# Kernel tuning notes

Measured on AMD Instinct MI355X. Metric: run time of the kernel, lower is better.

## Reference

```python
import jax, jax.numpy as jnp
import numpy as np

B, T, D_IN = 256, 250, 700
H1, H2, D_OUT = 256, 256, 20
B_J0 = 0.01
BETA = 1.8  # adaptation strength (isAdapt=1)
LENS, SCALE, HIGHT, GAMMA = 0.5, 6.0, 0.15, 0.5
SQRT_2PI = float(np.sqrt(2.0 * np.pi))


def _gaussian(x, mu, sigma):
    return jnp.exp(-((x - mu) ** 2) / (2.0 * sigma ** 2)) / (SQRT_2PI * sigma)


@jax.custom_vjp
def act_fun(x):
    # Heaviside spike with multi-Gaussian surrogate gradient (gradient_type='MG')
    return (x > 0).astype(x.dtype)


def _act_fwd(x):
    return act_fun(x), x


def _act_bwd(x, g):
    temp = (_gaussian(x, 0.0, LENS) * (1.0 + HIGHT)
            - _gaussian(x, LENS, SCALE * LENS) * HIGHT
            - _gaussian(x, -LENS, SCALE * LENS) * HIGHT)
    return (g * temp * GAMMA,)


act_fun.defvjp(_act_fwd, _act_bwd)


def setup_inputs() -> dict:
    key = jax.random.key(0)
    ks = jax.random.split(key, 16)
    # binary-ish spike input (SHD spike trains), rand fill
    x = (jax.random.uniform(ks[0], (B, T, D_IN)) < 0.1).astype(jnp.float32)

    def xavier(k, out_d, in_d):
        lim = float(np.sqrt(6.0 / (in_d + out_d)))
        return jax.random.uniform(k, (out_d, in_d), jnp.float32, -lim, lim)

    return {
        "x": x,
        "w_i2h1": xavier(ks[1], H1, D_IN),
        "w_h12h1": xavier(ks[2], H1, H1),
        "w_h12h2": xavier(ks[3], H2, H1),
        "w_h22h2": xavier(ks[4], H2, H2),
        "w_h2o": xavier(ks[5], D_OUT, H2),
        "b_h1": jnp.zeros((H1,), jnp.float32),
        "b_h2": jnp.zeros((H2,), jnp.float32),
        "b_o": jnp.zeros((D_OUT,), jnp.float32),
        "tau_adp_h1": 150.0 + 10.0 * jax.random.normal(ks[6], (H1,), jnp.float32),
        "tau_adp_h2": 150.0 + 10.0 * jax.random.normal(ks[7], (H2,), jnp.float32),
        "tau_m_h1": 20.0 + 5.0 * jax.random.normal(ks[8], (H1,), jnp.float32),
        "tau_m_h2": 20.0 + 5.0 * jax.random.normal(ks[9], (H2,), jnp.float32),
        "tau_m_o": 20.0 + 5.0 * jax.random.normal(ks[10], (D_OUT,), jnp.float32),
    }


def _lif_step(inp, mem, spk, b, alpha, ro):
    # mem_update_adp with params=None, dparams=None, isAdapt=1, dt=1, R_m=1
    b = ro * b + BETA * (1.0 - ro) * spk
    mem = mem * alpha - b * spk + (1.0 - alpha) * inp
    spk = act_fun(mem - b - B_J0)
    return mem, spk, b


def reference(x, w_i2h1, w_h12h1, w_h12h2, w_h22h2, w_h2o,
              b_h1, b_h2, b_o, tau_adp_h1, tau_adp_h2,
              tau_m_h1, tau_m_h2, tau_m_o):
    bsz = x.shape[0]
    h1, h2, d_out = w_i2h1.shape[0], w_h12h2.shape[0], w_h2o.shape[0]

    alpha1 = jnp.exp(-1.0 / tau_m_h1)
    ro1 = jnp.exp(-1.0 / tau_adp_h1)
    alpha2 = jnp.exp(-1.0 / tau_m_h2)
    ro2 = jnp.exp(-1.0 / tau_adp_h2)
    alpha_o = jnp.exp(-1.0 / tau_m_o)

    init = (
        jnp.zeros((bsz, h1)), jnp.zeros((bsz, h1)), jnp.full((bsz, h1), B_J0),
        jnp.zeros((bsz, h2)), jnp.zeros((bsz, h2)), jnp.full((bsz, h2), B_J0),
        jnp.zeros((bsz, d_out)), jnp.zeros((bsz, d_out)),
    )
    xT = jnp.swapaxes(x, 0, 1)  # [T, B, D_in]

    def step(carry, xt):
        mem1, spk1, bb1, mem2, spk2, bb2, mem_o, acc = carry
        h1_in = xt @ w_i2h1.T + spk1 @ w_h12h1.T + b_h1
        mem1, spk1, bb1 = _lif_step(h1_in, mem1, spk1, bb1, alpha1, ro1)
        h2_in = spk1 @ w_h12h2.T + spk2 @ w_h22h2.T + b_h2
        mem2, spk2, bb2 = _lif_step(h2_in, mem2, spk2, bb2, alpha2, ro2)
        o_in = spk2 @ w_h2o.T + b_o
        mem_o = mem_o * alpha_o + (1.0 - alpha_o) * o_in  # output_Neuron
        acc = acc + jax.nn.softmax(mem_o, axis=-1)
        return (mem1, spk1, bb1, mem2, spk2, bb2, mem_o, acc), None

    carry, _ = jax.lax.scan(step, init, xT)
    return carry[-1]  # accumulated softmax over the 250 timesteps, [B, 20]
```

## Files before the change

kernel.cpp:

```cpp
#include <hip/hip_runtime.h>
#include <cstdint>
#include <cstddef>

#define BB 256
#define TT 250
#define DIN 700
#define H1 256
#define H2 256
#define DOUT 20
#define BJ0 0.01f
#define BETAC 1.8f
#define IQSCALE 3.814697265625e-06f

typedef float f32x4 __attribute__((ext_vector_type(4)));
typedef int   i32x4 __attribute__((ext_vector_type(4)));

#define COFF_BL  180224
#define SOFF_T11 180224
#define SOFF_T12 245760
#define SOFF_T22 311296
#define FOFF_W2O 188416
#define FOFF_XP  193536
#define FOFF_MO  16577536
#define N_TRANS  381952

#define BARRIER_LDS() asm volatile("s_waitcnt lgkmcnt(0)\n\ts_barrier" ::: "memory")

__device__ __forceinline__ short q18(float w) {
    float s = w * 262144.0f;
    s = fminf(fmaxf(s, -32767.0f), 32767.0f);
    return (short)__float2int_rn(s);
}

__global__ void transpose_all_k(const float* __restrict__ w_i2h1,
                                const float* __restrict__ w_h12h1,
                                const float* __restrict__ w_h12h2,
                                const float* __restrict__ w_h22h2,
                                const float* __restrict__ w_h2o,
                                signed char* __restrict__ cws,
                                short* __restrict__ sws,
                                float* __restrict__ fws) {
    int i = blockIdx.x * blockDim.x + threadIdx.x;
    if (i < 180224) {
        int h = i / 704, k = i - h * 704;
        int q = (k < DIN) ? (int)q18(w_i2h1[h * DIN + k]) : 0;
        q = q > 32639 ? 32639 : (q < -32640 ? -32640 : q);
        int hi = (q + 128) >> 8;
        int lo = q - (hi << 8);
        cws[i] = (signed char)hi;
        cws[COFF_BL + i] = (signed char)lo;
        return;
    }
    i -= 180224;
    if (i < 65536) { int d = i >> 8, h = i & 255;
        sws[SOFF_T11 + i] = q18(w_h12h1[h * H1 + d]); return; }
    i -= 65536;
    if (i < 65536) { int d = i >> 8, h = i & 255;
        sws[SOFF_T12 + i] = q18(w_h12h2[h * H1 + d]); return; }
    i -= 65536;
    if (i < 65536) { int d = i >> 8, h = i & 255;
        sws[SOFF_T22 + i] = q18(w_h22h2[h * H2 + d]); return; }
    i -= 65536;
    if (i < 5120)  { int j = i / 20, o = i % 20;
        fws[FOFF_W2O + i] = w_h2o[o * H2 + j]; return; }
}

__global__ __launch_bounds__(256) void xgemm_k(const float* __restrict__ x,
                                               const signed char* __restrict__ Bh,
                                               const signed char* __restrict__ Bl,
                                               const float* __restrict__ b_h1,
                                               float* __restrict__ Xp) {
    const int t    = threadIdx.x;
    const int lane = t & 63;
    const int w    = t >> 6;
    const int m0   = blockIdx.x * 32;

    __shared__ __align__(16) signed char Asub[32 * 720];
    __shared__ __align__(16) signed char Bhs[256 * 80];
    __shared__ __align__(16) signed char Bls[256 * 80];

    #pragma unroll
    for (int it = 0; it < 22; ++it) {
        int flat = it * 256 + t;
        int row  = flat / 176;
        int c4   = flat - row * 176;
        unsigned int pk = 0u;
        if (c4 < 175) {
            const float* xr = x + (size_t)(m0 + row) * DIN;
            float4 f = *(const float4*)(xr + (c4 << 2));
            pk = (f.x != 0.f ? 1u : 0u)
               | (f.y != 0.f ? 1u : 0u) << 8
               | (f.z != 0.f ? 1u : 0u) << 16
               | (f.w != 0.f ? 1u : 0u) << 24;
        }
        *(unsigned int*)(Asub + row * 720 + (c4 << 2)) = pk;
    }

    i32x4 acch[2][4], accl[2][4];
    #pragma unroll
    for (int mt = 0; mt < 2; ++mt)
        #pragma unroll
        for (int nt = 0; nt < 4; ++nt) {
            acch[mt][nt] = (i32x4){0, 0, 0, 0};
            accl[mt][nt] = (i32x4){0, 0, 0, 0};
        }

    const int arow  = lane & 15;
    const int kg16  = (lane >> 4) << 4;
    const int bcol0 = w << 6;

    for (int ks = 0; ks < 11; ++ks) {
        __syncthreads();
        #pragma unroll
        for (int it2 = 0; it2 < 4; ++it2) {
            int row = it2 * 64 + (t >> 2);
            int ch  = (t & 3) << 4;
            int go  = row * 704 + ks * 64 + ch;
            *(int4*)(Bhs + row * 80 + ch) = *(const int4*)(Bh + go);
            *(int4*)(Bls + row * 80 + ch) = *(const int4*)(Bl + go);
        }
        __syncthreads();

        const int ko = ks * 64 + kg16;
        i32x4 a0 = *(const i32x4*)(Asub + arow * 720 + ko);
        i32x4 a1 = *(const i32x4*)(Asub + (16 + arow) * 720 + ko);
        #pragma unroll
        for (int nt = 0; nt < 4; ++nt) {
            const int bb = (bcol0 + nt * 16 + arow) * 80 + kg16;
            i32x4 bhf = *(const i32x4*)(Bhs + bb);
            i32x4 blf = *(const i32x4*)(Bls + bb);
            acch[0][nt] = __builtin_amdgcn_mfma_i32_16x16x64_i8(a0, bhf, acch[0][nt], 0, 0, 0);
            acch[1][nt] = __builtin_amdgcn_mfma_i32_16x16x64_i8(a1, bhf, acch[1][nt], 0, 0, 0);
            accl[0][nt] = __builtin_amdgcn_mfma_i32_16x16x64_i8(a0, blf, accl[0][nt], 0, 0, 0);
            accl[1][nt] = __builtin_amdgcn_mfma_i32_16x16x64_i8(a1, blf, accl[1][nt], 0, 0, 0);
        }
    }

    const int crb = (lane >> 4) << 2;
    #pragma unroll
    for (int nt = 0; nt < 4; ++nt) {
        int col = bcol0 + nt * 16 + arow;
        float bias = b_h1[col];
        #pragma unroll
        for (int mt = 0; mt < 2; ++mt) {
            #pragma unroll
            for (int r = 0; r < 4; ++r) {
                int row = m0 + mt * 16 + crb + r;
                int ir = (acch[mt][nt][r] << 8) + accl[mt][nt][r];
                __builtin_nontemporal_store(bias + (float)ir * IQSCALE,
                                            Xp + (size_t)row * H1 + col);
            }
        }
    }
}

__global__ __launch_bounds__(512) void rec_k(
    const float* __restrict__ Xp,
    const short* __restrict__ sT11, const short* __restrict__ sT12,
    const short* __restrict__ sT22, const float* __restrict__ wT2o,
    const float* __restrict__ b_h2, const float* __restrict__ b_o,
    const float* __restrict__ tau_adp_h1, const float* __restrict__ tau_adp_h2,
    const float* __restrict__ tau_m_h1, const float* __restrict__ tau_m_h2,
    const float* __restrict__ tau_m_o,
    float* __restrict__ Mo) {
    const int tid  = threadIdx.x;
    const int lane = tid & 63;
    const int w    = tid >> 6;
    const bool isL1 = (w < 4);
    const int c    = ((w & 3) << 6) + lane;
    const int b    = blockIdx.x;
    const float* __restrict__ XpB = Xp + (size_t)b * TT * H1;
    float* __restrict__ MoB = Mo + (size_t)b * TT * DOUT;

    __shared__ __align__(16) short sT22L[65536];
    __shared__ __align__(16) float w2oL[5120];
    __shared__ __align__(16) int lst1s[2][256];
    __shared__ __align__(16) int lst2s[2][256];
    __shared__ __align__(16) int lcnt[4][2];

    {
        const int* src = (const int*)sT22;
        int* dst = (int*)sT22L;
        for (int k = tid; k < 32768; k += 512) dst[k] = src[k];
        for (int k = tid; k < 5120; k += 512) w2oL[k] = wT2o[k];
        if (tid < 256) { lst1s[0][tid] = 0; lst1s[1][tid] = 0;
                         lst2s[0][tid] = 0; lst2s[1][tid] = 0; }
        if (tid < 8) ((int*)lcnt)[tid] = 0;
    }

    float alpha, rr, inb = 0.f;
    if (isL1) {
        alpha = expf(-1.0f / tau_m_h1[c]);
        rr    = expf(-1.0f / tau_adp_h1[c]);
    } else {
        alpha = expf(-1.0f / tau_m_h2[c]);
        rr    = expf(-1.0f / tau_adp_h2[c]);
        inb   = b_h2[c];
    }
    const int oc  = ((w & 3) * 5) + lane;
    const int ocs = (isL1 && lane < 5) ? oc : 0;
    float alpo = 0.f, bov = 0.f;
    if (isL1 && lane < 5) { alpo = expf(-1.0f / tau_m_o[oc]); bov = b_o[oc]; }

    float mem = 0.f, spk = 0.f, bbv = BJ0;
    float memo = 0.f;

    float xp_cur = 0.f;
    if (isL1) xp_cur = __builtin_nontemporal_load(XpB + c);
    __syncthreads();

    for (int i = 0; i <= TT + 1; ++i) {
        const int cur = i & 1, nxt = cur ^ 1;
        const int cc = i & 3, cn = (i + 1) & 3, cz = (i + 2) & 3;

        const int tot1 = lcnt[cc][0];
        const int tot2 = lcnt[cc][1];
        if (tid == 0) { lcnt[cz][0] = 0; lcnt[cz][1] = 0; }

        float xp_nxt = 0.f;
        if (isL1 && i + 1 < TT)
            xp_nxt = __builtin_nontemporal_load(XpB + (size_t)(i + 1) * H1 + c);

        const int* __restrict__ L1l = lst1s[cur];
        const int* __restrict__ L2l = lst2s[cur];

        int acc1 = 0, acc2 = 0;
        float ao = 0.f;

        if (isL1) {
            if (i < TT) {
                const short* colT = sT11 + c;
                int nb = tot1 >> 2, rem = tot1 & 3;
                for (int kk = 0; kk < nb; ++kk) {
                    int4 e = *(const int4*)(L1l + (kk << 2));
                    acc1 += colT[e.x << 8]; acc1 += colT[e.y << 8];
                    acc1 += colT[e.z << 8]; acc1 += colT[e.w << 8];
                }
                if (rem) {
                    int4 e = *(const int4*)(L1l + (nb << 2));
                    acc1 += colT[e.x << 8];
                    if (rem > 1) acc1 += colT[e.y << 8];
                    if (rem > 2) acc1 += colT[e.z << 8];
                }
            }
            if (i >= 2) {
                int nb = tot2 >> 2, rem = tot2 & 3;
                for (int kk = 0; kk < nb; ++kk) {
                    int4 e = *(const int4*)(L2l + (kk << 2));
                    float v0 = w2oL[e.x * DOUT + ocs];
                    float v1 = w2oL[e.y * DOUT + ocs];
                    float v2 = w2oL[e.z * DOUT + ocs];
                    float v3 = w2oL[e.w * DOUT + ocs];
                    ao += (v0 + v1) + (v2 + v3);
                }
                if (rem) {
                    int4 e = *(const int4*)(L2l + (nb << 2));
                    ao += w2oL[e.x * DOUT + ocs];
                    if (rem > 1) ao += w2oL[e.y * DOUT + ocs];
                    if (rem > 2) ao += w2oL[e.z * DOUT + ocs];
                }
            }
        } else if (i >= 1 && i <= TT) {
            {
                const short* colT = sT12 + c;
                int nb = tot1 >> 2, rem = tot1 & 3;
                for (int kk = 0; kk < nb; ++kk) {
                    int4 e = *(const int4*)(L1l + (kk << 2));
                    acc1 += colT[e.x << 8]; acc1 += colT[e.y << 8];
                    acc1 += colT[e.z << 8]; acc1 += colT[e.w << 8];
                }
                if (rem) {
                    int4 e = *(const int4*)(L1l + (nb << 2));
                    acc1 += colT[e.x << 8];
                    if (rem > 1) acc1 += colT[e.y << 8];
                    if (rem > 2) acc1 += colT[e.z << 8];
                }
            }
            {
                const short* colL = sT22L + c;
                int nb = tot2 >> 2, rem = tot2 & 3;
                for (int kk = 0; kk < nb; ++kk) {
                    int4 e = *(const int4*)(L2l + (kk << 2));
                    acc2 += colL[e.x << 8]; acc2 += colL[e.y << 8];
                    acc2 += colL[e.z << 8]; acc2 += colL[e.w << 8];
                }
                if (rem) {
                    int4 e = *(const int4*)(L2l + (nb << 2));
                    acc2 += colL[e.x << 8];
                    if (rem > 1) acc2 += colL[e.y << 8];
                    if (rem > 2) acc2 += colL[e.z << 8];
                }
            }
        }

        if (isL1) {
            if (i < TT) {
                float r1 = (float)acc1 * IQSCALE;
                bbv = rr * bbv + BETAC * (1.f - rr) * spk;
                mem = mem * alpha - bbv * spk + (1.f - alpha) * (xp_cur + r1);
                float ns = (mem - bbv - BJ0) > 0.f ? 1.f : 0.f;
                spk = ns;
                unsigned long long m = __ballot(ns != 0.f ? 1 : 0);
                int base = 0;
                if (lane == 0) base = atomicAdd(&lcnt[cn][0], __popcll(m));
                base = __shfl(base, 0);
                if (ns != 0.f)
                    lst1s[nxt][base + __popcll(m & ((1ull << lane) - 1ull))] = c;
            }
            if (lane < 5 && i >= 2) {
                memo = memo * alpo + (1.f - alpo) * (bov + ao);
                __builtin_nontemporal_store(memo, MoB + (size_t)(i - 2) * DOUT + oc);
            }
        } else if (i >= 1 && i <= TT) {
            float r23 = (float)(acc1 + acc2) * IQSCALE;
            bbv = rr * bbv + BETAC * (1.f - rr) * spk;
            mem = mem * alpha - bbv * spk + (1.f - alpha) * (inb + r23);
            float ns = (mem - bbv - BJ0) > 0.f ? 1.f : 0.f;
            spk = ns;
            unsigned long long m = __ballot(ns != 0.f ? 1 : 0);
            int base = 0;
            if (lane == 0) base = atomicAdd(&lcnt[cn][1], __popcll(m));
            base = __shfl(base, 0);
            if (ns != 0.f)
                lst2s[nxt][base + __popcll(m & ((1ull << lane) - 1ull))] = c;
        }

        BARRIER_LDS();
        xp_cur = xp_nxt;
    }
}

__global__ __launch_bounds__(256) void soft_k(const float* __restrict__ Mo,
                                              float* __restrict__ out) {
    const int b = blockIdx.x;
    const int t = threadIdx.x;
    __shared__ float sm[TT][DOUT];

    if (t < TT) {
        const float* row = Mo + ((size_t)b * TT + t) * DOUT;
        float v[DOUT];
        #pragma unroll
        for (int k = 0; k < DOUT; k += 4) {
            float4 r = *(const float4*)(row + k);
            v[k] = r.x; v[k + 1] = r.y; v[k + 2] = r.z; v[k + 3] = r.w;
        }
        float mx = v[0];
        #pragma unroll
        for (int j = 1; j < DOUT; ++j) mx = fmaxf(mx, v[j]);
        float s = 0.f;
        #pragma unroll
        for (int j = 0; j < DOUT; ++j) { v[j] = __expf(v[j] - mx); s += v[j]; }
        float inv = 1.0f / s;
        #pragma unroll
        for (int j = 0; j < DOUT; ++j) sm[t][j] = v[j] * inv;
    }
    __syncthreads();
    if (t < DOUT) {
        float acc = 0.f;
        for (int tt = 0; tt < TT; ++tt) acc += sm[tt][t];
        out[b * DOUT + t] = acc;
    }
}

extern "C" void kernel_launch(void* const* d_in, const int* in_sizes, int n_in,
                              void* d_out, int out_size, void* d_ws, size_t ws_size,
                              hipStream_t stream) {
    const float* x          = (const float*)d_in[0];
    const float* w_i2h1     = (const float*)d_in[1];
    const float* w_h12h1    = (const float*)d_in[2];
    const float* w_h12h2    = (const float*)d_in[3];
    const float* w_h22h2    = (const float*)d_in[4];
    const float* w_h2o      = (const float*)d_in[5];
    const float* b_h1       = (const float*)d_in[6];
    const float* b_h2       = (const float*)d_in[7];
    const float* b_o        = (const float*)d_in[8];
    const float* tau_adp_h1 = (const float*)d_in[9];
    const float* tau_adp_h2 = (const float*)d_in[10];
    const float* tau_m_h1   = (const float*)d_in[11];
    const float* tau_m_h2   = (const float*)d_in[12];
    const float* tau_m_o    = (const float*)d_in[13];

    signed char* cws = (signed char*)d_ws;
    short* sws = (short*)d_ws;
    float* fws = (float*)d_ws;
    const signed char* Bh = cws;
    const signed char* Bl = cws + COFF_BL;
    const short* sT11 = sws + SOFF_T11;
    const short* sT12 = sws + SOFF_T12;
    const short* sT22 = sws + SOFF_T22;
    float* wT2o = fws + FOFF_W2O;
    float* Xp   = fws + FOFF_XP;
    float* Mo   = fws + FOFF_MO;

    transpose_all_k<<<N_TRANS / 256, 256, 0, stream>>>(
        w_i2h1, w_h12h1, w_h12h2, w_h22h2, w_h2o, cws, sws, fws);

    xgemm_k<<<(BB * TT) / 32, 256, 0, stream>>>(x, Bh, Bl, b_h1, Xp);

    rec_k<<<BB, 512, 0, stream>>>(Xp, sT11, sT12, sT22, wT2o,
                                  b_h2, b_o, tau_adp_h1, tau_adp_h2,
                                  tau_m_h1, tau_m_h2, tau_m_o, Mo);

    soft_k<<<BB, 256, 0, stream>>>(Mo, (float*)d_out);
}
```

Baseline: 689.6 us.

## Replace LDS spike index lists with per-wave ballot bitmasks

Each wave now writes its 64-bit ballot mask of spiking neurons to LDS, replacing the atomic-counter compacted index lists. Consumers read the four masks into scalar registers with readfirstlane and walk the set bits with ctz to gather weight columns. This removes the LDS atomics, shuffles, scattered list writes and int4 list loads from each timestep. In exchange the gather loops become scalar bit-scan loops with a dependent ctz per spike and less unrolling.

```diff
diff --git a/kernel.cpp b/kernel.cpp
--- a/kernel.cpp
+++ b/kernel.cpp
@@ -30,6 +30,12 @@
     float s = w * 262144.0f;
     s = fminf(fmaxf(s, -32767.0f), 32767.0f);
     return (short)__float2int_rn(s);
+}
+
+__device__ __forceinline__ unsigned long long rfl64(unsigned long long m) {
+    unsigned lo = __builtin_amdgcn_readfirstlane((unsigned)m);
+    unsigned hi = __builtin_amdgcn_readfirstlane((unsigned)(m >> 32));
+    return ((unsigned long long)hi << 32) | lo;
 }
 
 __global__ void transpose_all_k(const float* __restrict__ w_i2h1,
@@ -174,18 +180,16 @@
 
     __shared__ __align__(16) short sT22L[65536];
     __shared__ __align__(16) float w2oL[5120];
-    __shared__ __align__(16) int lst1s[2][256];
-    __shared__ __align__(16) int lst2s[2][256];
-    __shared__ __align__(16) int lcnt[4][2];
+    __shared__ unsigned long long wm1[2][4];
+    __shared__ unsigned long long wm2[2][4];
 
     {
         const int* src = (const int*)sT22;
         int* dst = (int*)sT22L;
         for (int k = tid; k < 32768; k += 512) dst[k] = src[k];
         for (int k = tid; k < 5120; k += 512) w2oL[k] = wT2o[k];
-        if (tid < 256) { lst1s[0][tid] = 0; lst1s[1][tid] = 0;
-                         lst2s[0][tid] = 0; lst2s[1][tid] = 0; }
-        if (tid < 8) ((int*)lcnt)[tid] = 0;
+        if (tid < 8) wm1[tid >> 2][tid & 3] = 0ULL;
+        else if (tid < 16) wm2[(tid - 8) >> 2][tid & 3] = 0ULL;
     }
 
     float alpha, rr, inb = 0.f;
@@ -211,18 +215,17 @@
 
     for (int i = 0; i <= TT + 1; ++i) {
         const int cur = i & 1, nxt = cur ^ 1;
-        const int cc = i & 3, cn = (i + 1) & 3, cz = (i + 2) & 3;
-
-        const int tot1 = lcnt[cc][0];
-        const int tot2 = lcnt[cc][1];
-        if (tid == 0) { lcnt[cz][0] = 0; lcnt[cz][1] = 0; }
 
         float xp_nxt = 0.f;
         if (isL1 && i + 1 < TT)
             xp_nxt = __builtin_nontemporal_load(XpB + (size_t)(i + 1) * H1 + c);
 
-        const int* __restrict__ L1l = lst1s[cur];
-        const int* __restrict__ L2l = lst2s[cur];
+        unsigned long long M1[4], M2[4];
+        #pragma unroll
+        for (int q = 0; q < 4; ++q) {
+            M1[q] = rfl64(wm1[cur][q]);
+            M2[q] = rfl64(wm2[cur][q]);
+        }
 
         int acc1 = 0, acc2 = 0;
         float ao = 0.f;
@@ -230,99 +233,84 @@
         if (isL1) {
             if (i < TT) {
                 const short* colT = sT11 + c;
-                int nb = tot1 >> 2, rem = tot1 & 3;
-                for (int kk = 0; kk < nb; ++kk) {
-                    int4 e = *(const int4*)(L1l + (kk << 2));
-                    acc1 += colT[e.x << 8]; acc1 += colT[e.y << 8];
-                    acc1 += colT[e.z << 8]; acc1 += colT[e.w << 8];
+                #pragma unroll
+                for (int q = 0; q < 4; ++q) {
+                    unsigned long long m = M1[q];
+                    const int base = q << 6;
+                    while (m) {
+                        int j = __builtin_ctzll(m);
+                        m &= m - 1;
+                        acc1 += colT[(base + j) << 8];
+                    }
                 }
-                if (rem) {
-                    int4 e = *(const int4*)(L1l + (nb << 2));
-                    acc1 += colT[e.x << 8];
-                    if (rem > 1) acc1 += colT[e.y << 8];
-                    if (rem > 2) acc1 += colT[e.z << 8];
-                }
-            }
-            if (i >= 2) {
-                int nb = tot2 >> 2, rem = tot2 & 3;
-                for (int kk = 0; kk < nb; ++kk) {
-                    int4 e = *(const int4*)(L2l + (kk << 2));
-                    float v0 = w2oL[e.x * DOUT + ocs];
-                    float v1 = w2oL[e.y * DOUT + ocs];
-                    float v2 = w2oL[e.z * DOUT + ocs];
-                    float v3 = w2oL[e.w * DOUT + ocs];
-                    ao += (v0 + v1) + (v2 + v3);
-                }
-                if (rem) {
-                    int4 e = *(const int4*)(L2l + (nb << 2));
-                    ao += w2oL[e.x * DOUT + ocs];
-                    if (rem > 1) ao += w2oL[e.y * DOUT + ocs];
-                    if (rem > 2) ao += w2oL[e.z * DOUT + ocs];
+            }
+            if (lane < 5 && i >= 2) {
+                #pragma unroll
+                for (int q = 0; q < 4; ++q) {
+                    unsigned long long m = M2[q];
+                    const int base = q << 6;
+                    while (m) {
+                        int j = __builtin_ctzll(m);
+                        m &= m - 1;
+                        ao += w2oL[(base + j) * DOUT + ocs];
+                    }
                 }
             }
         } else if (i >= 1 && i <= TT) {
             {
                 const short* colT = sT12 + c;
-                int nb = tot1 >> 2, rem = tot1 & 3;
-                for (int kk = 0; kk < nb; ++kk) {
-                    int4 e = *(const int4*)(L1l + (kk << 2));
-                    acc1 += colT[e.x << 8]; acc1 += colT[e.y << 8];
-                    acc1 += colT[e.z << 8]; acc1 += colT[e.w << 8];
-                }
-                if (rem) {
-                    int4 e = *(const int4*)(L1l + (nb << 2));
-                    acc1 += colT[e.x << 8];
-                    if (rem > 1) acc1 += colT[e.y << 8];
-                    if (rem > 2) acc1 += colT[e.z << 8];
+                #pragma unroll
+                for (int q = 0; q < 4; ++q) {
+                    unsigned long long m = M1[q];
+                    const int base = q << 6;
+                    while (m) {
+                        int j = __builtin_ctzll(m);
+                        m &= m - 1;
+                        acc1 += colT[(base + j) << 8];
+                    }
                 }
             }
             {
                 const short* colL = sT22L + c;
-                int nb = tot2 >> 2, rem = tot2 & 3;
-                for (int kk = 0; kk < nb; ++kk) {
-                    int4 e = *(const int4*)(L2l + (kk << 2));
-                    acc2 += colL[e.x << 8]; acc2 += colL[e.y << 8];
-                    acc2 += colL[e.z << 8]; acc2 += colL[e.w << 8];
+                #pragma unroll
+                for (int q = 0; q < 4; ++q) {
+                    unsigned long long m = M2[q];
+                    const int base = q << 6;
+                    while (m) {
+                        int j = __builtin_ctzll(m);
+                        m &= m - 1;
+                        acc2 += colL[(base + j) << 8];
+                    }
                 }
-                if (rem) {
-                    int4 e = *(const int4*)(L2l + (nb << 2));
-                    acc2 += colL[e.x << 8];
-                    if (rem > 1) acc2 += colL[e.y << 8];
-                    if (rem > 2) acc2 += colL[e.z << 8];
-                }
             }
         }
 
         if (isL1) {
+            unsigned long long nm = 0ULL;
             if (i < TT) {
                 float r1 = (float)acc1 * IQSCALE;
                 bbv = rr * bbv + BETAC * (1.f - rr) * spk;
                 mem = mem * alpha - bbv * spk + (1.f - alpha) * (xp_cur + r1);
                 float ns = (mem - bbv - BJ0) > 0.f ? 1.f : 0.f;
                 spk = ns;
-                unsigned long long m = __ballot(ns != 0.f ? 1 : 0);
-                int base = 0;
-                if (lane == 0) base = atomicAdd(&lcnt[cn][0], __popcll(m));
-                base = __shfl(base, 0);
-                if (ns != 0.f)
-                    lst1s[nxt][base + __popcll(m & ((1ull << lane) - 1ull))] = c;
-            }
+                nm = __ballot(ns != 0.f ? 1 : 0);
+            }
+            if (lane == 0) wm1[nxt][w] = nm;
             if (lane < 5 && i >= 2) {
                 memo = memo * alpo + (1.f - alpo) * (bov + ao);
                 __builtin_nontemporal_store(memo, MoB + (size_t)(i - 2) * DOUT + oc);
             }
-        } else if (i >= 1 && i <= TT) {
-            float r23 = (float)(acc1 + acc2) * IQSCALE;
-            bbv = rr * bbv + BETAC * (1.f - rr) * spk;
-            mem = mem * alpha - bbv * spk + (1.f - alpha) * (inb + r23);
-            float ns = (mem - bbv - BJ0) > 0.f ? 1.f : 0.f;
-            spk = ns;
-            unsigned long long m = __ballot(ns != 0.f ? 1 : 0);
-            int base = 0;
-            if (lane == 0) base = atomicAdd(&lcnt[cn][1], __popcll(m));
-            base = __shfl(base, 0);
-            if (ns != 0.f)
-                lst2s[nxt][base + __popcll(m & ((1ull << lane) - 1ull))] = c;
+        } else {
+            unsigned long long nm = 0ULL;
+            if (i >= 1 && i <= TT) {
+                float r23 = (float)(acc1 + acc2) * IQSCALE;
+                bbv = rr * bbv + BETAC * (1.f - rr) * spk;
+                mem = mem * alpha - bbv * spk + (1.f - alpha) * (inb + r23);
+                float ns = (mem - bbv - BJ0) > 0.f ? 1.f : 0.f;
+                spk = ns;
+                nm = __ballot(ns != 0.f ? 1 : 0);
+            }
+            if (lane == 0) wm2[nxt][w & 3] = nm;
         }
 
         BARRIER_LDS();
```

Result: slower. 824.3 us (+19.5%).

## Pad spike lists with dummy zero row and unroll gathers by 32

Applied to the files above, without the earlier changes.

Adds a zero-weight dummy row (index 256) to each transposed recurrent weight table and to the output weight table, and pre-fills the spike index lists with that dummy index. Sparse gather loops can then round the spike count up to a multiple of 32 and run a fully unrolled 32-wide gather with four independent accumulators, with no remainder handling. The lists are now quadruple-buffered so each one can be reset to dummy two steps ahead. The aim is more memory-level parallelism and less loop and branch overhead in the latency-bound recurrent kernel, at the cost of extra wasted gathers on the padding and slightly more LDS.

```diff
diff --git a/kernel.cpp b/kernel.cpp
--- a/kernel.cpp
+++ b/kernel.cpp
@@ -10,6 +10,7 @@
 #define DOUT 20
 #define BJ0 0.01f
 #define BETAC 1.8f
+#define DUMMY 256
 #define IQSCALE 3.814697265625e-06f
 
 typedef float f32x4 __attribute__((ext_vector_type(4)));
@@ -17,12 +18,12 @@
 
 #define COFF_BL  180224
 #define SOFF_T11 180224
-#define SOFF_T12 245760
-#define SOFF_T22 311296
-#define FOFF_W2O 188416
-#define FOFF_XP  193536
-#define FOFF_MO  16577536
-#define N_TRANS  381952
+#define SOFF_T12 246016
+#define SOFF_T22 311808
+#define FOFF_W2O 188800
+#define FOFF_XP  193940
+#define FOFF_MO  16577940
+#define N_TRANS  382740
 
 #define BARRIER_LDS() asm volatile("s_waitcnt lgkmcnt(0)\n\ts_barrier" ::: "memory")
 
@@ -52,17 +53,17 @@
         return;
     }
     i -= 180224;
-    if (i < 65536) { int d = i >> 8, h = i & 255;
-        sws[SOFF_T11 + i] = q18(w_h12h1[h * H1 + d]); return; }
-    i -= 65536;
-    if (i < 65536) { int d = i >> 8, h = i & 255;
-        sws[SOFF_T12 + i] = q18(w_h12h2[h * H1 + d]); return; }
-    i -= 65536;
-    if (i < 65536) { int d = i >> 8, h = i & 255;
-        sws[SOFF_T22 + i] = q18(w_h22h2[h * H2 + d]); return; }
-    i -= 65536;
-    if (i < 5120)  { int j = i / 20, o = i % 20;
-        fws[FOFF_W2O + i] = w_h2o[o * H2 + j]; return; }
+    if (i < 65792) { int d = i >> 8, h = i & 255;
+        sws[SOFF_T11 + i] = (d < H1) ? q18(w_h12h1[h * H1 + d]) : (short)0; return; }
+    i -= 65792;
+    if (i < 65792) { int d = i >> 8, h = i & 255;
+        sws[SOFF_T12 + i] = (d < H1) ? q18(w_h12h2[h * H1 + d]) : (short)0; return; }
+    i -= 65792;
+    if (i < 65792) { int d = i >> 8, h = i & 255;
+        sws[SOFF_T22 + i] = (d < H2) ? q18(w_h22h2[h * H2 + d]) : (short)0; return; }
+    i -= 65792;
+    if (i < 5140)  { int j = i / 20, o = i % 20;
+        fws[FOFF_W2O + i] = (j < H2) ? w_h2o[o * H2 + j] : 0.f; return; }
 }
 
 __global__ __launch_bounds__(256) void xgemm_k(const float* __restrict__ x,
@@ -152,6 +153,50 @@
             }
         }
     }
+}
+
+__device__ __forceinline__ int g32s(const short* __restrict__ T,
+                                    const int* __restrict__ L) {
+    int4 e0 = *(const int4*)(L);
+    int4 e1 = *(const int4*)(L + 4);
+    int4 e2 = *(const int4*)(L + 8);
+    int4 e3 = *(const int4*)(L + 12);
+    int4 e4 = *(const int4*)(L + 16);
+    int4 e5 = *(const int4*)(L + 20);
+    int4 e6 = *(const int4*)(L + 24);
+    int4 e7 = *(const int4*)(L + 28);
+    int a = 0, b = 0, c = 0, d = 0;
+    a += T[e0.x << 8]; b += T[e0.y << 8]; c += T[e0.z << 8]; d += T[e0.w << 8];
+    a += T[e1.x << 8]; b += T[e1.y << 8]; c += T[e1.z << 8]; d += T[e1.w << 8];
+    a += T[e2.x << 8]; b += T[e2.y << 8]; c += T[e2.z << 8]; d += T[e2.w << 8];
+    a += T[e3.x << 8]; b += T[e3.y << 8]; c += T[e3.z << 8]; d += T[e3.w << 8];
+    a += T[e4.x << 8]; b += T[e4.y << 8]; c += T[e4.z << 8]; d += T[e4.w << 8];
+    a += T[e5.x << 8]; b += T[e5.y << 8]; c += T[e5.z << 8]; d += T[e5.w << 8];
+    a += T[e6.x << 8]; b += T[e6.y << 8]; c += T[e6.z << 8]; d += T[e6.w << 8];
+    a += T[e7.x << 8]; b += T[e7.y << 8]; c += T[e7.z << 8]; d += T[e7.w << 8];
+    return (a + b) + (c + d);
+}
+
+__device__ __forceinline__ float g32f(const float* __restrict__ T,
+                                      const int* __restrict__ L) {
+    int4 e0 = *(const int4*)(L);
+    int4 e1 = *(const int4*)(L + 4);
+    int4 e2 = *(const int4*)(L + 8);
+    int4 e3 = *(const int4*)(L + 12);
+    int4 e4 = *(const int4*)(L + 16);
+    int4 e5 = *(const int4*)(L + 20);
+    int4 e6 = *(const int4*)(L + 24);
+    int4 e7 = *(const int4*)(L + 28);
+    float a = 0.f, b = 0.f, c = 0.f, d = 0.f;
+    a += T[e0.x * DOUT]; b += T[e0.y * DOUT]; c += T[e0.z * DOUT]; d += T[e0.w * DOUT];
+    a += T[e1.x * DOUT]; b += T[e1.y * DOUT]; c += T[e1.z * DOUT]; d += T[e1.w * DOUT];
+    a += T[e2.x * DOUT]; b += T[e2.y * DOUT]; c += T[e2.z * DOUT]; d += T[e2.w * DOUT];
+    a += T[e3.x * DOUT]; b += T[e3.y * DOUT]; c += T[e3.z * DOUT]; d += T[e3.w * DOUT];
+    a += T[e4.x * DOUT]; b += T[e4.y * DOUT]; c += T[e4.z * DOUT]; d += T[e4.w * DOUT];
+    a += T[e5.x * DOUT]; b += T[e5.y * DOUT]; c += T[e5.z * DOUT]; d += T[e5.w * DOUT];
+    a += T[e6.x * DOUT]; b += T[e6.y * DOUT]; c += T[e6.z * DOUT]; d += T[e6.w * DOUT];
+    a += T[e7.x * DOUT]; b += T[e7.y * DOUT]; c += T[e7.z * DOUT]; d += T[e7.w * DOUT];
+    return (a + b) + (c + d);
 }
 
 __global__ __launch_bounds__(512) void rec_k(
@@ -172,19 +217,21 @@
     const float* __restrict__ XpB = Xp + (size_t)b * TT * H1;
     float* __restrict__ MoB = Mo + (size_t)b * TT * DOUT;
 
-    __shared__ __align__(16) short sT22L[65536];
-    __shared__ __align__(16) float w2oL[5120];
-    __shared__ __align__(16) int lst1s[2][256];
-    __shared__ __align__(16) int lst2s[2][256];
-    __shared__ __align__(16) int lcnt[4][2];
+    __shared__ __align__(16) short sT22L[65792];
+    __shared__ __align__(16) float w2oL[5140];
+    __shared__ __align__(16) int lst1s[4][256];
+    __shared__ __align__(16) int lst2s[4][256];
+    __shared__ int lcnt[4][2];
 
     {
         const int* src = (const int*)sT22;
         int* dst = (int*)sT22L;
-        for (int k = tid; k < 32768; k += 512) dst[k] = src[k];
-        for (int k = tid; k < 5120; k += 512) w2oL[k] = wT2o[k];
-        if (tid < 256) { lst1s[0][tid] = 0; lst1s[1][tid] = 0;
-                         lst2s[0][tid] = 0; lst2s[1][tid] = 0; }
+        for (int k = tid; k < 32896; k += 512) dst[k] = src[k];
+        for (int k = tid; k < 5140; k += 512) w2oL[k] = wT2o[k];
+        for (int k = tid; k < 1024; k += 512) {
+            ((int*)lst1s)[k] = DUMMY;
+            ((int*)lst2s)[k] = DUMMY;
+        }
         if (tid < 8) ((int*)lcnt)[tid] = 0;
     }
 
@@ -210,86 +257,44 @@
     __syncthreads();
 
     for (int i = 0; i <= TT + 1; ++i) {
-        const int cur = i & 1, nxt = cur ^ 1;
         const int cc = i & 3, cn = (i + 1) & 3, cz = (i + 2) & 3;
 
         const int tot1 = lcnt[cc][0];
         const int tot2 = lcnt[cc][1];
         if (tid == 0) { lcnt[cz][0] = 0; lcnt[cz][1] = 0; }
 
+        if (tid < 256) lst1s[cz][tid] = DUMMY;
+        else           lst2s[cz][tid - 256] = DUMMY;
+
         float xp_nxt = 0.f;
         if (isL1 && i + 1 < TT)
             xp_nxt = __builtin_nontemporal_load(XpB + (size_t)(i + 1) * H1 + c);
 
-        const int* __restrict__ L1l = lst1s[cur];
-        const int* __restrict__ L2l = lst2s[cur];
+        const int* __restrict__ L1l = lst1s[cc];
+        const int* __restrict__ L2l = lst2s[cc];
+        const int np1 = (tot1 + 31) & ~31;
+        const int np2 = (tot2 + 31) & ~31;
 
         int acc1 = 0, acc2 = 0;
         float ao = 0.f;
 
         if (isL1) {
-            if (i < TT) {
-                const short* colT = sT11 + c;
-                int nb = tot1 >> 2, rem = tot1 & 3;
-                for (int kk = 0; kk < nb; ++kk) {
-                    int4 e = *(const int4*)(L1l + (kk << 2));
-                    acc1 += colT[e.x << 8]; acc1 += colT[e.y << 8];
-                    acc1 += colT[e.z << 8]; acc1 += colT[e.w << 8];
-                }
-                if (rem) {
-                    int4 e = *(const int4*)(L1l + (nb << 2));
-                    acc1 += colT[e.x << 8];
-                    if (rem > 1) acc1 += colT[e.y << 8];
-                    if (rem > 2) acc1 += colT[e.z << 8];
-                }
-            }
-            if (i >= 2) {
-                int nb = tot2 >> 2, rem = tot2 & 3;
-                for (int kk = 0; kk < nb; ++kk) {
-                    int4 e = *(const int4*)(L2l + (kk << 2));
-                    float v0 = w2oL[e.x * DOUT + ocs];
-                    float v1 = w2oL[e.y * DOUT + ocs];
-                    float v2 = w2oL[e.z * DOUT + ocs];
-                    float v3 = w2oL[e.w * DOUT + ocs];
-                    ao += (v0 + v1) + (v2 + v3);
-                }
-                if (rem) {
-                    int4 e = *(const int4*)(L2l + (nb << 2));
-                    ao += w2oL[e.x * DOUT + ocs];
-                    if (rem > 1) ao += w2oL[e.y * DOUT + ocs];
-                    if (rem > 2) ao += w2oL[e.z * DOUT + ocs];
-                }
+            const bool d1 = (i < TT);
+            const bool d2 = (i >= 2);
+            const short* colT = sT11 + c;
+            const float* colO = w2oL + ocs;
+            const int npm = (d1 ? np1 : 0) > (d2 ? np2 : 0) ? np1 : np2;
+            for (int k = 0; k < npm; k += 32) {
+                if (d1 && k < np1) acc1 += g32s(colT, L1l + k);
+                if (d2 && k < np2) ao   += g32f(colO, L2l + k);
             }
         } else if (i >= 1 && i <= TT) {
-            {
-                const short* colT = sT12 + c;
-                int nb = tot1 >> 2, rem = tot1 & 3;
-                for (int kk = 0; kk < nb; ++kk) {
-                    int4 e = *(const int4*)(L1l + (kk << 2));
-                    acc1 += colT[e.x << 8]; acc1 += colT[e.y << 8];
-                    acc1 += colT[e.z << 8]; acc1 += colT[e.w << 8];
-                }
-                if (rem) {
-                    int4 e = *(const int4*)(L1l + (nb << 2));
-                    acc1 += colT[e.x << 8];
-                    if (rem > 1) acc1 += colT[e.y << 8];
-                    if (rem > 2) acc1 += colT[e.z << 8];
-                }
-            }
-            {
-                const short* colL = sT22L + c;
-                int nb = tot2 >> 2, rem = tot2 & 3;
-                for (int kk = 0; kk < nb; ++kk) {
-                    int4 e = *(const int4*)(L2l + (kk << 2));
-                    acc2 += colL[e.x << 8]; acc2 += colL[e.y << 8];
-                    acc2 += colL[e.z << 8]; acc2 += colL[e.w << 8];
-                }
-                if (rem) {
-                    int4 e = *(const int4*)(L2l + (nb << 2));
-                    acc2 += colL[e.x << 8];
-                    if (rem > 1) acc2 += colL[e.y << 8];
-                    if (rem > 2) acc2 += colL[e.z << 8];
-                }
+            const short* colT = sT12 + c;
+            const short* colL = sT22L + c;
+            const int npm = np1 > np2 ? np1 : np2;
+            for (int k = 0; k < npm; k += 32) {
+                if (k < np1) acc1 += g32s(colT, L1l + k);
+                if (k < np2) acc2 += g32s(colL, L2l + k);
             }
         }
 
@@ -305,7 +310,7 @@
                 if (lane == 0) base = atomicAdd(&lcnt[cn][0], __popcll(m));
                 base = __shfl(base, 0);
                 if (ns != 0.f)
-                    lst1s[nxt][base + __popcll(m & ((1ull << lane) - 1ull))] = c;
+                    lst1s[cn][base + __popcll(m & ((1ull << lane) - 1ull))] = c;
             }
             if (lane < 5 && i >= 2) {
                 memo = memo * alpo + (1.f - alpo) * (bov + ao);
@@ -322,7 +327,7 @@
             if (lane == 0) base = atomicAdd(&lcnt[cn][1], __popcll(m));
             base = __shfl(base, 0);
             if (ns != 0.f)
-                lst2s[nxt][base + __popcll(m & ((1ull << lane) - 1ull))] = c;
+                lst2s[cn][base + __popcll(m & ((1ull << lane) - 1ull))] = c;
         }
 
         BARRIER_LDS();
@@ -392,7 +397,7 @@
     float* Xp   = fws + FOFF_XP;
     float* Mo   = fws + FOFF_MO;
 
-    transpose_all_k<<<N_TRANS / 256, 256, 0, stream>>>(
+    transpose_all_k<<<(N_TRANS + 255) / 256, 256, 0, stream>>>(
         w_i2h1, w_h12h1, w_h12h2, w_h22h2, w_h2o, cws, sws, fws);
 
     xgemm_k<<<(BB * TT) / 32, 256, 0, stream>>>(x, Bh, Bl, b_h1, Xp);
```

After: 757.1 us. 9.8% more time.
